# Kernel tuning notes

Hardware: AMD Instinct MI355X
Metric: run time of the kernel (lower is better)

The kernel has to match this reference:

```python
import jax, jax.numpy as jnp
import numpy as np

N_HEAD = 8
C = 32
M_DIM = 256
N_SEQ = 256
L_RES = 384
SQ_C = 1.0 / np.sqrt(C)


def setup_inputs() -> dict:
    key = jax.random.key(0)
    ks = jax.random.split(key, 10)
    hc = N_HEAD * C
    s = 0.02
    return {
        "m": jax.random.normal(ks[0], (N_SEQ, L_RES, M_DIM), dtype=jnp.float32),
        "ln_gamma": jnp.ones((M_DIM,), jnp.float32),
        "ln_beta": jnp.zeros((M_DIM,), jnp.float32),
        "Wq": jax.random.normal(ks[1], (M_DIM, hc), jnp.float32) * s,
        "Wk": jax.random.normal(ks[2], (M_DIM, hc), jnp.float32) * s,
        "Wv": jax.random.normal(ks[3], (M_DIM, hc), jnp.float32) * s,
        "Wg": jax.random.normal(ks[4], (M_DIM, hc), jnp.float32) * s,
        "bg": jnp.zeros((hc,), jnp.float32),
        "Wo": jax.random.normal(ks[5], (hc, M_DIM), jnp.float32) * s,
        "bo": jnp.zeros((M_DIM,), jnp.float32),
    }


def layer_norm(x, gamma, beta, eps=1e-5):
    mu = jnp.mean(x, axis=-1, keepdims=True)
    var = jnp.var(x, axis=-1, keepdims=True)
    return (x - mu) * jax.lax.rsqrt(var + eps) * gamma + beta


def reference(m, ln_gamma, ln_beta, Wq, Wk, Wv, Wg, bg, Wo, bo):
    N, L, D = m.shape
    x = layer_norm(m, ln_gamma, ln_beta)
    q = (x @ Wq).reshape(N, L, N_HEAD, C)
    k = (x @ Wk).reshape(N, L, N_HEAD, C)
    v = (x @ Wv).reshape(N, L, N_HEAD, C)
    g = jax.nn.sigmoid(x @ Wg + bg).reshape(N, L, N_HEAD, C)
    # attention over the sequence axis (s,t), independent per column l, head h
    att = jnp.einsum('slhc,tlhc->stlh', q, k) * SQ_C
    att = jax.nn.softmax(att, axis=1)
    o = jnp.einsum('stlh,tlhc->slhc', att, v) * g
    return o.reshape(N, L, N_HEAD * C) @ Wo + bo
```

## Files before the change

### kernel.cpp

```cpp
#include <hip/hip_runtime.h>
#include <cstdint>
#include <cstddef>

#define NSEQ 256
#define LRES 384
#define MDIM 256
#define NHEAD 8
#define CDIM 32
#define NL (NSEQ*LRES)
#define SQC 0.17677669529663687f

#define X_OFF    0u
#define WT_OFF   25165824u
#define QKVG_OFF 25493504u
#define PROJ_SZ  25165824u
#define O_OFF    (QKVG_OFF + 4u*PROJ_SZ)

typedef __attribute__((ext_vector_type(8))) __bf16 bf16x8;
typedef __attribute__((ext_vector_type(4))) float f32x4;

__device__ __forceinline__ unsigned short f2bf(float f) {
  unsigned int u = __float_as_uint(f);
  u = (u + 0x7FFFu + ((u >> 16) & 1u)) >> 16;
  return (unsigned short)u;
}
__device__ __forceinline__ unsigned short f2bf_fast(float f) {
  return (unsigned short)((__float_as_uint(f) + 0x8000u) >> 16);
}
__device__ __forceinline__ float bf2f(unsigned short u){ return __uint_as_float(((unsigned int)u) << 16); }

__global__ __launch_bounds__(256) void ln_kernel(const float* __restrict__ m,
    const float* __restrict__ gamma, const float* __restrict__ beta,
    unsigned short* __restrict__ x)
{
  int row  = blockIdx.x*4 + (threadIdx.x >> 6);
  int lane = threadIdx.x & 63;
  const float4 v = ((const float4*)(m + (size_t)row*MDIM))[lane];
  float s  = v.x + v.y + v.z + v.w;
  float ss = v.x*v.x + v.y*v.y + v.z*v.z + v.w*v.w;
  #pragma unroll
  for (int off = 32; off > 0; off >>= 1) {
    s  += __shfl_xor(s,  off, 64);
    ss += __shfl_xor(ss, off, 64);
  }
  float mu   = s * (1.f/MDIM);
  float var  = ss * (1.f/MDIM) - mu*mu;
  float rstd = rsqrtf(var + 1e-5f);
  float4 gm = ((const float4*)gamma)[lane];
  float4 bt = ((const float4*)beta)[lane];
  ushort4 pk;
  pk.x = f2bf((v.x - mu)*rstd*gm.x + bt.x);
  pk.y = f2bf((v.y - mu)*rstd*gm.y + bt.y);
  pk.z = f2bf((v.z - mu)*rstd*gm.z + bt.z);
  pk.w = f2bf((v.w - mu)*rstd*gm.w + bt.w);
  ((ushort4*)(x + (size_t)row*MDIM))[lane] = pk;
}

__global__ __launch_bounds__(256) void wtr_kernel(
    const float* __restrict__ W0, const float* __restrict__ W1,
    const float* __restrict__ W2, const float* __restrict__ W3,
    const float* __restrict__ W4, unsigned short* __restrict__ wT)
{
  int p = blockIdx.z;
  const float* W = (p==0)?W0:(p==1)?W1:(p==2)?W2:(p==3)?W3:W4;
  __shared__ float tile[32][33];
  int tx = threadIdx.x & 31, ty0 = threadIdx.x >> 5;
  int bi = blockIdx.x*32, bj = blockIdx.y*32;
  #pragma unroll
  for (int r = 0; r < 4; r++) {
    int ty = ty0 + r*8;
    tile[ty][tx] = W[(bi + ty)*MDIM + bj + tx];
  }
  __syncthreads();
  #pragma unroll
  for (int r = 0; r < 4; r++) {
    int ty = ty0 + r*8;
    wT[p*65536 + (bj + ty)*MDIM + bi + tx] = f2bf(tile[tx][ty]);
  }
}

__global__ __launch_bounds__(256) void proj_kernel(const unsigned short* __restrict__ x,
    const unsigned short* __restrict__ wT, const float* __restrict__ bg,
    unsigned short* __restrict__ qkvg)
{
  __shared__ __align__(16) unsigned short As[128*32];
  __shared__ __align__(16) unsigned short Bs[64*32];
  const int bn = blockIdx.x, bm = blockIdx.y;
  const int tid = threadIdx.x;
  const int lane = tid & 63, wave = tid >> 6;
  const int ln = lane & 15, quad = lane >> 4;
  const int wm = (wave >> 1)*64, wn = (wave & 1)*32;
  const int Rbase = bm*128, Nbase = bn*64;
  const uint4* xg = (const uint4*)x;
  const uint4* wg = (const uint4*)wT;
  uint4* Asv = (uint4*)As;
  uint4* Bsv = (uint4*)Bs;
  const int aRow0 = tid >> 2, aCol = tid & 3;
  const int J0 = Nbase + (tid >> 2);
  const int bIdxBase = (J0 >> 8)*8192 + (J0 & 255)*32 + (tid & 3);

  f32x4 zero = {0.f, 0.f, 0.f, 0.f};
  f32x4 acc[4][2];
  #pragma unroll
  for (int i=0;i<4;i++)
    #pragma unroll
    for (int j=0;j<2;j++) acc[i][j] = zero;

  for (int kk = 0; kk < 8; kk++) {
    Asv[tid]       = xg[(Rbase + aRow0)*32      + kk*4 + aCol];
    Asv[tid + 256] = xg[(Rbase + aRow0 + 64)*32 + kk*4 + aCol];
    Bsv[tid]       = wg[bIdxBase + kk*4];
    __syncthreads();
    bf16x8 af[4], bf[2];
    #pragma unroll
    for (int i=0;i<4;i++) af[i] = __builtin_bit_cast(bf16x8, Asv[(wm + i*16 + ln)*4 + quad]);
    #pragma unroll
    for (int j=0;j<2;j++) bf[j] = __builtin_bit_cast(bf16x8, Bsv[(wn + j*16 + ln)*4 + quad]);
    #pragma unroll
    for (int i=0;i<4;i++)
      #pragma unroll
      for (int j=0;j<2;j++)
        acc[i][j] = __builtin_amdgcn_mfma_f32_16x16x32_bf16(af[i], bf[j], acc[i][j], 0, 0, 0);
    __syncthreads();
  }

  const int p = Nbase >> 8;
  const int sIdx = Rbase / 384;
  const int l0 = Rbase - sIdx*384;
  unsigned short* dstBase = qkvg + (size_t)p*PROJ_SZ;
  #pragma unroll
  for (int i=0;i<4;i++) {
    #pragma unroll
    for (int j=0;j<2;j++) {
      int Jc = Nbase + wn + j*16 + ln;
      int j256 = Jc & 255;
      int h = j256 >> 5, c = j256 & 31;
      #pragma unroll
      for (int r=0;r<4;r++) {
        int row = wm + i*16 + quad*4 + r;
        int lcol = l0 + row;
        float val = acc[i][j][r];
        if (p == 3) val = 1.f/(1.f + __expf(-(val + bg[j256])));
        dstBase[(size_t)((lcol*8 + h)*256 + sIdx)*32 + c] = f2bf(val);
      }
    }
  }
}

__global__ __launch_bounds__(256) void vtr_kernel(const unsigned short* __restrict__ v,
    unsigned short* __restrict__ vt)
{
  __shared__ unsigned short tile[32][33];
  const int lh = blockIdx.y, st = blockIdx.x;
  const unsigned short* src = v  + (size_t)lh*8192;
  unsigned short*       dst = vt + (size_t)lh*8192;
  int tx = threadIdx.x & 31, ty0 = threadIdx.x >> 5;
  #pragma unroll
  for (int r=0;r<4;r++) {
    int ty = ty0 + r*8;
    tile[ty][tx] = src[(st*32 + ty)*32 + tx];
  }
  __syncthreads();
  #pragma unroll
  for (int r=0;r<4;r++) {
    int ty = ty0 + r*8;
    dst[ty*256 + st*32 + tx] = tile[tx][ty];
  }
}

__global__ __launch_bounds__(256, 2) void attn_kernel(
    const unsigned short* __restrict__ qkvg,
    const unsigned short* __restrict__ vt,
    unsigned short* __restrict__ o)
{
  const int h = blockIdx.x, l = blockIdx.y;
  const int tid = threadIdx.x;
  const int wave = tid >> 6, lane = tid & 63;
  const int ln = lane & 15, qd = lane >> 4;
  __shared__ __align__(16) unsigned short Pa[16384];
  const size_t tb = (size_t)(l*8 + h) * 8192;
  const uint4* qg = (const uint4*)qkvg + (tb >> 3);
  const uint4* kg = (const uint4*)(qkvg + (size_t)PROJ_SZ) + (tb >> 3);
  const uint4* vg = (const uint4*)vt + (tb >> 3);
  const int s0 = wave*64;
  const int sw = ln & 7;

  bf16x8 qf[4];
  #pragma unroll
  for (int nj=0;nj<4;nj++)
    qf[nj] = __builtin_bit_cast(bf16x8, qg[(s0 + ln + 16*nj)*4 + qd]);

  f32x4 zero = {0.f,0.f,0.f,0.f};
  f32x4 Oacc[2][4];
  #pragma unroll
  for (int mi=0;mi<2;mi++)
    #pragma unroll
    for (int nj=0;nj<4;nj++) Oacc[mi][nj] = zero;
  float rs[4] = {0.f,0.f,0.f,0.f};

  ushort4* Paw = (ushort4*)Pa;
  const uint4* Pa4 = (const uint4*)Pa;
  const int wbw = wave*1024;
  const int wb4 = wave*512;

  for (int c = 0; c < 4; c++) {
    bf16x8 kf[4];
    uint4 vfr[2][2];
    #pragma unroll
    for (int mi=0;mi<4;mi++)
      kf[mi] = __builtin_bit_cast(bf16x8, kg[(c*64 + 16*mi + ln)*4 + qd]);
    #pragma unroll
    for (int mi=0;mi<2;mi++)
      #pragma unroll
      for (int ks=0;ks<2;ks++)
        vfr[mi][ks] = vg[(ln + 16*mi)*32 + c*8 + ks*4 + qd];

    #pragma unroll
    for (int nj=0;nj<4;nj++) {
      f32x4 sv[4];
      #pragma unroll
      for (int mi=0;mi<4;mi++)
        sv[mi] = __builtin_amdgcn_mfma_f32_16x16x32_bf16(kf[mi], qf[nj], zero, 0, 0, 0);
      const int srow = ln + 16*nj;
      #pragma unroll
      for (int mi=0;mi<4;mi++) {
        float p0 = __expf(sv[mi][0]*SQC);
        float p1 = __expf(sv[mi][1]*SQC);
        float p2 = __expf(sv[mi][2]*SQC);
        float p3 = __expf(sv[mi][3]*SQC);
        rs[nj] += (p0+p1)+(p2+p3);
        ushort4 pk;
        pk.x = f2bf_fast(p0); pk.y = f2bf_fast(p1);
        pk.z = f2bf_fast(p2); pk.w = f2bf_fast(p3);
        Paw[wbw + srow*16 + (((2*mi + (qd>>1)) ^ sw) << 1) + (qd & 1)] = pk;
      }
    }
    #pragma unroll
    for (int ks=0;ks<2;ks++) {
      bf16x8 pf[4];
      #pragma unroll
      for (int nj=0;nj<4;nj++)
        pf[nj] = __builtin_bit_cast(bf16x8, Pa4[wb4 + (ln + 16*nj)*8 + ((4*ks + qd) ^ sw)]);
      #pragma unroll
      for (int mi=0;mi<2;mi++)
        #pragma unroll
        for (int nj=0;nj<4;nj++)
          Oacc[mi][nj] = __builtin_amdgcn_mfma_f32_16x16x32_bf16(
              __builtin_bit_cast(bf16x8, vfr[mi][ks]), pf[nj], Oacc[mi][nj], 0, 0, 0);
    }
  }

  #pragma unroll
  for (int nj=0;nj<4;nj++) {
    float r = rs[nj];
    r += __shfl_xor(r, 16, 64);
    r += __shfl_xor(r, 32, 64);
    rs[nj] = 1.f / r;
  }

  const unsigned short* gg = qkvg + 3u*(size_t)PROJ_SZ + tb;
  #pragma unroll
  for (int mi=0;mi<2;mi++) {
    #pragma unroll
    for (int nj=0;nj<4;nj++) {
      const int sg = s0 + ln + 16*nj;
      const int c0 = 16*mi + 4*qd;
      ushort4 gv = *(const ushort4*)(gg + sg*32 + c0);
      float inv = rs[nj];
      float o0 = Oacc[mi][nj][0] * inv * bf2f(gv.x);
      float o1 = Oacc[mi][nj][1] * inv * bf2f(gv.y);
      float o2 = Oacc[mi][nj][2] * inv * bf2f(gv.z);
      float o3 = Oacc[mi][nj][3] * inv * bf2f(gv.w);
      ushort4 ov;
      ov.x = f2bf(o0); ov.y = f2bf(o1); ov.z = f2bf(o2); ov.w = f2bf(o3);
      *(ushort4*)(o + ((size_t)(sg*LRES + l)*8 + h)*32 + c0) = ov;
    }
  }
}

__global__ __launch_bounds__(256) void out_kernel(const unsigned short* __restrict__ o,
    const unsigned short* __restrict__ wT, const float* __restrict__ bo,
    float* __restrict__ out)
{
  __shared__ __align__(16) unsigned short As[128*32];
  __shared__ __align__(16) unsigned short Bs[64*32];
  const int bn = blockIdx.x, bm = blockIdx.y;
  const int tid = threadIdx.x;
  const int lane = tid & 63, wave = tid >> 6;
  const int ln = lane & 15, quad = lane >> 4;
  const int wm = (wave >> 1)*64, wn = (wave & 1)*32;
  const int Rbase = bm*128, Nbase = bn*64;
  const uint4* og = (const uint4*)o;
  const uint4* wg = (const uint4*)wT;
  uint4* Asv = (uint4*)As;
  uint4* Bsv = (uint4*)Bs;
  const int aRow0 = tid >> 2, aCol = tid & 3;
  const int J0 = Nbase + (tid >> 2);
  const int bIdxBase = 32768 + J0*32 + (tid & 3);

  f32x4 zero = {0.f, 0.f, 0.f, 0.f};
  f32x4 acc[4][2];
  #pragma unroll
  for (int i=0;i<4;i++)
    #pragma unroll
    for (int j=0;j<2;j++) acc[i][j] = zero;

  for (int kk = 0; kk < 8; kk++) {
    Asv[tid]       = og[(Rbase + aRow0)*32      + kk*4 + aCol];
    Asv[tid + 256] = og[(Rbase + aRow0 + 64)*32 + kk*4 + aCol];
    Bsv[tid]       = wg[bIdxBase + kk*4];
    __syncthreads();
    bf16x8 af[4], bf[2];
    #pragma unroll
    for (int i=0;i<4;i++) af[i] = __builtin_bit_cast(bf16x8, Asv[(wm + i*16 + ln)*4 + quad]);
    #pragma unroll
    for (int j=0;j<2;j++) bf[j] = __builtin_bit_cast(bf16x8, Bsv[(wn + j*16 + ln)*4 + quad]);
    #pragma unroll
    for (int i=0;i<4;i++)
      #pragma unroll
      for (int j=0;j<2;j++)
        acc[i][j] = __builtin_amdgcn_mfma_f32_16x16x32_bf16(af[i], bf[j], acc[i][j], 0, 0, 0);
    __syncthreads();
  }

  #pragma unroll
  for (int i=0;i<4;i++) {
    #pragma unroll
    for (int j=0;j<2;j++) {
      int Jc = Nbase + wn + j*16 + ln;
      float bias = bo[Jc];
      #pragma unroll
      for (int r=0;r<4;r++) {
        int row = wm + i*16 + quad*4 + r;
        out[(size_t)(Rbase + row)*256 + Jc] = acc[i][j][r] + bias;
      }
    }
  }
}

extern "C" void kernel_launch(void* const* d_in, const int* in_sizes, int n_in,
                              void* d_out, int out_size, void* d_ws, size_t ws_size,
                              hipStream_t stream)
{
  const float* m     = (const float*)d_in[0];
  const float* gamma = (const float*)d_in[1];
  const float* beta  = (const float*)d_in[2];
  const float* Wq    = (const float*)d_in[3];
  const float* Wk    = (const float*)d_in[4];
  const float* Wv    = (const float*)d_in[5];
  const float* Wg    = (const float*)d_in[6];
  const float* bg    = (const float*)d_in[7];
  const float* Wo    = (const float*)d_in[8];
  const float* bo    = (const float*)d_in[9];
  float* out = (float*)d_out;
  unsigned short* ws   = (unsigned short*)d_ws;
  unsigned short* x    = ws + X_OFF;
  unsigned short* wT   = ws + WT_OFF;
  unsigned short* qkvg = ws + QKVG_OFF;
  unsigned short* ob   = ws + O_OFF;
  unsigned short* vnat = qkvg + 2u*(size_t)PROJ_SZ;

  hipLaunchKernelGGL(ln_kernel,   dim3(NL/4),      dim3(256), 0, stream, m, gamma, beta, x);
  hipLaunchKernelGGL(wtr_kernel,  dim3(8, 8, 5),   dim3(256), 0, stream, Wq, Wk, Wv, Wg, Wo, wT);
  hipLaunchKernelGGL(proj_kernel, dim3(16, 768),   dim3(256), 0, stream, x, wT, bg, qkvg);
  hipLaunchKernelGGL(vtr_kernel,  dim3(8, 3072),   dim3(256), 0, stream, vnat, x);
  hipLaunchKernelGGL(attn_kernel, dim3(8, 384),    dim3(256), 0, stream, qkvg, x, ob);
  hipLaunchKernelGGL(out_kernel,  dim3(4, 768),    dim3(256), 0, stream, ob, wT, bo, out);
}
```

Baseline: 483.7 us.

## Enlarge GEMM tiles with direct global-to-LDS loads and row-major projection output

The projection and output GEMMs move to 128x128 tiles with a K-step of 64, loading through global_load_lds into an XOR-swizzled LDS layout instead of staging through registers. The projection now writes Q/K/V/G in natural row-major order rather than scattering into a per-(l,h) layout. The V transpose and attention kernels gather strided rows from that layout instead. The attention grid is reordered so adjacent blocks share the same head. This aims to cut GEMM load overhead and the scattered projection stores, at the cost of strided, less coalesced reads in attention.

```diff
diff --git a/kernel.cpp b/kernel.cpp
--- a/kernel.cpp
+++ b/kernel.cpp
@@ -28,6 +28,12 @@
   return (unsigned short)((__float_as_uint(f) + 0x8000u) >> 16);
 }
 __device__ __forceinline__ float bf2f(unsigned short u){ return __uint_as_float(((unsigned int)u) << 16); }
+
+__device__ __forceinline__ void gld16(const void* g, void* l) {
+  __builtin_amdgcn_global_load_lds(
+      (const __attribute__((address_space(1))) unsigned int*)g,
+      (__attribute__((address_space(3))) unsigned int*)l, 16, 0, 0);
+}
 
 __global__ __launch_bounds__(256) void ln_kernel(const float* __restrict__ m,
     const float* __restrict__ gamma, const float* __restrict__ beta,
@@ -83,65 +89,77 @@
     const unsigned short* __restrict__ wT, const float* __restrict__ bg,
     unsigned short* __restrict__ qkvg)
 {
-  __shared__ __align__(16) unsigned short As[128*32];
-  __shared__ __align__(16) unsigned short Bs[64*32];
+  __shared__ __align__(16) unsigned short As[128*64];
+  __shared__ __align__(16) unsigned short Bs[128*64];
   const int bn = blockIdx.x, bm = blockIdx.y;
   const int tid = threadIdx.x;
   const int lane = tid & 63, wave = tid >> 6;
-  const int ln = lane & 15, quad = lane >> 4;
-  const int wm = (wave >> 1)*64, wn = (wave & 1)*32;
-  const int Rbase = bm*128, Nbase = bn*64;
-  const uint4* xg = (const uint4*)x;
-  const uint4* wg = (const uint4*)wT;
-  uint4* Asv = (uint4*)As;
-  uint4* Bsv = (uint4*)Bs;
-  const int aRow0 = tid >> 2, aCol = tid & 3;
-  const int J0 = Nbase + (tid >> 2);
-  const int bIdxBase = (J0 >> 8)*8192 + (J0 & 255)*32 + (tid & 3);
-
-  f32x4 zero = {0.f, 0.f, 0.f, 0.f};
-  f32x4 acc[4][2];
+  const int ln = lane & 15, qd = lane >> 4;
+  const int wm = (wave >> 1)*64, wn = (wave & 1)*64;
+  const int Rbase = bm*128, Nbase = bn*128;
+
+  const int row0 = tid >> 3;
+  const int kc   = (tid & 7) ^ (row0 & 7);
+  const unsigned short* aS = x + (size_t)(Rbase + row0)*256 + kc*8;
+  const unsigned short* bS = wT + (size_t)(bn >> 1)*65536
+                           + (size_t)((bn & 1)*128 + row0)*256 + kc*8;
+  unsigned short* ldsA = As + wave*512;
+  unsigned short* ldsB = Bs + wave*512;
+
+  f32x4 zero = {0.f,0.f,0.f,0.f};
+  f32x4 acc[4][4];
   #pragma unroll
   for (int i=0;i<4;i++)
     #pragma unroll
-    for (int j=0;j<2;j++) acc[i][j] = zero;
-
-  for (int kk = 0; kk < 8; kk++) {
-    Asv[tid]       = xg[(Rbase + aRow0)*32      + kk*4 + aCol];
-    Asv[tid + 256] = xg[(Rbase + aRow0 + 64)*32 + kk*4 + aCol];
-    Bsv[tid]       = wg[bIdxBase + kk*4];
+    for (int j=0;j<4;j++) acc[i][j] = zero;
+
+  const uint4* As4 = (const uint4*)As;
+  const uint4* Bs4 = (const uint4*)Bs;
+
+  for (int kk = 0; kk < 4; kk++) {
+    #pragma unroll
+    for (int e = 0; e < 4; e++) {
+      gld16(aS + e*8192, ldsA + e*2048);
+      gld16(bS + e*8192, ldsB + e*2048);
+    }
+    aS += 64; bS += 64;
     __syncthreads();
-    bf16x8 af[4], bf[2];
-    #pragma unroll
-    for (int i=0;i<4;i++) af[i] = __builtin_bit_cast(bf16x8, Asv[(wm + i*16 + ln)*4 + quad]);
-    #pragma unroll
-    for (int j=0;j<2;j++) bf[j] = __builtin_bit_cast(bf16x8, Bsv[(wn + j*16 + ln)*4 + quad]);
-    #pragma unroll
-    for (int i=0;i<4;i++)
-      #pragma unroll
-      for (int j=0;j<2;j++)
-        acc[i][j] = __builtin_amdgcn_mfma_f32_16x16x32_bf16(af[i], bf[j], acc[i][j], 0, 0, 0);
+    #pragma unroll
+    for (int kh = 0; kh < 2; kh++) {
+      bf16x8 af[4], bfr[4];
+      #pragma unroll
+      for (int i=0;i<4;i++) {
+        int r = wm + i*16 + ln;
+        af[i] = __builtin_bit_cast(bf16x8, As4[r*8 + ((kh*4 + qd) ^ (r & 7))]);
+      }
+      #pragma unroll
+      for (int j=0;j<4;j++) {
+        int r = wn + j*16 + ln;
+        bfr[j] = __builtin_bit_cast(bf16x8, Bs4[r*8 + ((kh*4 + qd) ^ (r & 7))]);
+      }
+      #pragma unroll
+      for (int i=0;i<4;i++)
+        #pragma unroll
+        for (int j=0;j<4;j++)
+          acc[i][j] = __builtin_amdgcn_mfma_f32_16x16x32_bf16(af[i], bfr[j], acc[i][j], 0, 0, 0);
+    }
     __syncthreads();
   }
 
   const int p = Nbase >> 8;
-  const int sIdx = Rbase / 384;
-  const int l0 = Rbase - sIdx*384;
   unsigned short* dstBase = qkvg + (size_t)p*PROJ_SZ;
   #pragma unroll
   for (int i=0;i<4;i++) {
     #pragma unroll
-    for (int j=0;j<2;j++) {
+    for (int j=0;j<4;j++) {
       int Jc = Nbase + wn + j*16 + ln;
       int j256 = Jc & 255;
-      int h = j256 >> 5, c = j256 & 31;
       #pragma unroll
       for (int r=0;r<4;r++) {
-        int row = wm + i*16 + quad*4 + r;
-        int lcol = l0 + row;
+        int row = Rbase + wm + i*16 + qd*4 + r;
         float val = acc[i][j][r];
         if (p == 3) val = 1.f/(1.f + __expf(-(val + bg[j256])));
-        dstBase[(size_t)((lcol*8 + h)*256 + sIdx)*32 + c] = f2bf(val);
+        dstBase[(size_t)row*256 + j256] = f2bf(val);
       }
     }
   }
@@ -151,20 +169,20 @@
     unsigned short* __restrict__ vt)
 {
   __shared__ unsigned short tile[32][33];
-  const int lh = blockIdx.y, st = blockIdx.x;
-  const unsigned short* src = v  + (size_t)lh*8192;
-  unsigned short*       dst = vt + (size_t)lh*8192;
+  const int st = blockIdx.x;
+  const int lh = blockIdx.y;
+  const int l = lh >> 3, h = lh & 7;
   int tx = threadIdx.x & 31, ty0 = threadIdx.x >> 5;
   #pragma unroll
   for (int r=0;r<4;r++) {
     int ty = ty0 + r*8;
-    tile[ty][tx] = src[(st*32 + ty)*32 + tx];
+    tile[ty][tx] = v[((size_t)(st*32 + ty)*384 + l)*256 + h*32 + tx];
   }
   __syncthreads();
   #pragma unroll
   for (int r=0;r<4;r++) {
     int ty = ty0 + r*8;
-    dst[ty*256 + st*32 + tx] = tile[tx][ty];
+    vt[(size_t)lh*8192 + ty*256 + st*32 + tx] = tile[tx][ty];
   }
 }
 
@@ -173,22 +191,22 @@
     const unsigned short* __restrict__ vt,
     unsigned short* __restrict__ o)
 {
-  const int h = blockIdx.x, l = blockIdx.y;
+  const int l = blockIdx.x, h = blockIdx.y;
   const int tid = threadIdx.x;
   const int wave = tid >> 6, lane = tid & 63;
   const int ln = lane & 15, qd = lane >> 4;
   __shared__ __align__(16) unsigned short Pa[16384];
-  const size_t tb = (size_t)(l*8 + h) * 8192;
-  const uint4* qg = (const uint4*)qkvg + (tb >> 3);
-  const uint4* kg = (const uint4*)(qkvg + (size_t)PROJ_SZ) + (tb >> 3);
-  const uint4* vg = (const uint4*)vt + (tb >> 3);
+  const uint4* qg = (const uint4*)qkvg;
+  const uint4* kg = qg + (size_t)PROJ_SZ/8;
+  const uint4* vg = (const uint4*)vt + (size_t)(l*8 + h)*1024;
+  const int hq = h*4;
   const int s0 = wave*64;
   const int sw = ln & 7;
 
   bf16x8 qf[4];
   #pragma unroll
   for (int nj=0;nj<4;nj++)
-    qf[nj] = __builtin_bit_cast(bf16x8, qg[(s0 + ln + 16*nj)*4 + qd]);
+    qf[nj] = __builtin_bit_cast(bf16x8, qg[((size_t)(s0 + ln + 16*nj)*384 + l)*32 + hq + qd]);
 
   f32x4 zero = {0.f,0.f,0.f,0.f};
   f32x4 Oacc[2][4];
@@ -208,7 +226,7 @@
     uint4 vfr[2][2];
     #pragma unroll
     for (int mi=0;mi<4;mi++)
-      kf[mi] = __builtin_bit_cast(bf16x8, kg[(c*64 + 16*mi + ln)*4 + qd]);
+      kf[mi] = __builtin_bit_cast(bf16x8, kg[((size_t)(c*64 + 16*mi + ln)*384 + l)*32 + hq + qd]);
     #pragma unroll
     for (int mi=0;mi<2;mi++)
       #pragma unroll
@@ -258,22 +276,22 @@
     rs[nj] = 1.f / r;
   }
 
-  const unsigned short* gg = qkvg + 3u*(size_t)PROJ_SZ + tb;
+  const unsigned short* gg = qkvg + 3u*(size_t)PROJ_SZ;
   #pragma unroll
   for (int mi=0;mi<2;mi++) {
     #pragma unroll
     for (int nj=0;nj<4;nj++) {
       const int sg = s0 + ln + 16*nj;
       const int c0 = 16*mi + 4*qd;
-      ushort4 gv = *(const ushort4*)(gg + sg*32 + c0);
+      const size_t rowOff = ((size_t)sg*384 + l)*256 + h*32 + c0;
+      ushort4 gv = *(const ushort4*)(gg + rowOff);
       float inv = rs[nj];
-      float o0 = Oacc[mi][nj][0] * inv * bf2f(gv.x);
-      float o1 = Oacc[mi][nj][1] * inv * bf2f(gv.y);
-      float o2 = Oacc[mi][nj][2] * inv * bf2f(gv.z);
-      float o3 = Oacc[mi][nj][3] * inv * bf2f(gv.w);
       ushort4 ov;
-      ov.x = f2bf(o0); ov.y = f2bf(o1); ov.z = f2bf(o2); ov.w = f2bf(o3);
-      *(ushort4*)(o + ((size_t)(sg*LRES + l)*8 + h)*32 + c0) = ov;
+      ov.x = f2bf(Oacc[mi][nj][0] * inv * bf2f(gv.x));
+      ov.y = f2bf(Oacc[mi][nj][1] * inv * bf2f(gv.y));
+      ov.z = f2bf(Oacc[mi][nj][2] * inv * bf2f(gv.z));
+      ov.w = f2bf(Oacc[mi][nj][3] * inv * bf2f(gv.w));
+      *(ushort4*)(o + rowOff) = ov;
     }
   }
 }
@@ -282,57 +300,72 @@
     const unsigned short* __restrict__ wT, const float* __restrict__ bo,
     float* __restrict__ out)
 {
-  __shared__ __align__(16) unsigned short As[128*32];
-  __shared__ __align__(16) unsigned short Bs[64*32];
+  __shared__ __align__(16) unsigned short As[128*64];
+  __shared__ __align__(16) unsigned short Bs[128*64];
   const int bn = blockIdx.x, bm = blockIdx.y;
   const int tid = threadIdx.x;
   const int lane = tid & 63, wave = tid >> 6;
-  const int ln = lane & 15, quad = lane >> 4;
-  const int wm = (wave >> 1)*64, wn = (wave & 1)*32;
-  const int Rbase = bm*128, Nbase = bn*64;
-  const uint4* og = (const uint4*)o;
-  const uint4* wg = (const uint4*)wT;
-  uint4* Asv = (uint4*)As;
-  uint4* Bsv = (uint4*)Bs;
-  const int aRow0 = tid >> 2, aCol = tid & 3;
-  const int J0 = Nbase + (tid >> 2);
-  const int bIdxBase = 32768 + J0*32 + (tid & 3);
-
-  f32x4 zero = {0.f, 0.f, 0.f, 0.f};
-  f32x4 acc[4][2];
+  const int ln = lane & 15, qd = lane >> 4;
+  const int wm = (wave >> 1)*64, wn = (wave & 1)*64;
+  const int Rbase = bm*128, Nbase = bn*128;
+
+  const int row0 = tid >> 3;
+  const int kc   = (tid & 7) ^ (row0 & 7);
+  const unsigned short* aS = o  + (size_t)(Rbase + row0)*256 + kc*8;
+  const unsigned short* bS = wT + 4u*65536 + (size_t)(Nbase + row0)*256 + kc*8;
+  unsigned short* ldsA = As + wave*512;
+  unsigned short* ldsB = Bs + wave*512;
+
+  f32x4 zero = {0.f,0.f,0.f,0.f};
+  f32x4 acc[4][4];
   #pragma unroll
   for (int i=0;i<4;i++)
     #pragma unroll
-    for (int j=0;j<2;j++) acc[i][j] = zero;
-
-  for (int kk = 0; kk < 8; kk++) {
-    Asv[tid]       = og[(Rbase + aRow0)*32      + kk*4 + aCol];
-    Asv[tid + 256] = og[(Rbase + aRow0 + 64)*32 + kk*4 + aCol];
-    Bsv[tid]       = wg[bIdxBase + kk*4];
+    for (int j=0;j<4;j++) acc[i][j] = zero;
+
+  const uint4* As4 = (const uint4*)As;
+  const uint4* Bs4 = (const uint4*)Bs;
+
+  for (int kk = 0; kk < 4; kk++) {
+    #pragma unroll
+    for (int e = 0; e < 4; e++) {
+      gld16(aS + e*8192, ldsA + e*2048);
+      gld16(bS + e*8192, ldsB + e*2048);
+    }
+    aS += 64; bS += 64;
     __syncthreads();
-    bf16x8 af[4], bf[2];
-    #pragma unroll
-    for (int i=0;i<4;i++) af[i] = __builtin_bit_cast(bf16x8, Asv[(wm + i*16 + ln)*4 + quad]);
-    #pragma unroll
-    for (int j=0;j<2;j++) bf[j] = __builtin_bit_cast(bf16x8, Bsv[(wn + j*16 + ln)*4 + quad]);
-    #pragma unroll
-    for (int i=0;i<4;i++)
-      #pragma unroll
-      for (int j=0;j<2;j++)
-        acc[i][j] = __builtin_amdgcn_mfma_f32_16x16x32_bf16(af[i], bf[j], acc[i][j], 0, 0, 0);
+    #pragma unroll
+    for (int kh = 0; kh < 2; kh++) {
+      bf16x8 af[4], bfr[4];
+      #pragma unroll
+      for (int i=0;i<4;i++) {
+        int r = wm + i*16 + ln;
+        af[i] = __builtin_bit_cast(bf16x8, As4[r*8 + ((kh*4 + qd) ^ (r & 7))]);
+      }
+      #pragma unroll
+      for (int j=0;j<4;j++) {
+        int r = wn + j*16 + ln;
+        bfr[j] = __builtin_bit_cast(bf16x8, Bs4[r*8 + ((kh*4 + qd) ^ (r & 7))]);
+      }
+      #pragma unroll
+      for (int i=0;i<4;i++)
+        #pragma unroll
+        for (int j=0;j<4;j++)
+          acc[i][j] = __builtin_amdgcn_mfma_f32_16x16x32_bf16(af[i], bfr[j], acc[i][j], 0, 0, 0);
+    }
     __syncthreads();
   }
 
   #pragma unroll
   for (int i=0;i<4;i++) {
     #pragma unroll
-    for (int j=0;j<2;j++) {
+    for (int j=0;j<4;j++) {
       int Jc = Nbase + wn + j*16 + ln;
       float bias = bo[Jc];
       #pragma unroll
       for (int r=0;r<4;r++) {
-        int row = wm + i*16 + quad*4 + r;
-        out[(size_t)(Rbase + row)*256 + Jc] = acc[i][j][r] + bias;
+        int row = Rbase + wm + i*16 + qd*4 + r;
+        out[(size_t)row*256 + Jc] = acc[i][j][r] + bias;
       }
     }
   }
@@ -362,8 +395,8 @@
 
   hipLaunchKernelGGL(ln_kernel,   dim3(NL/4),      dim3(256), 0, stream, m, gamma, beta, x);
   hipLaunchKernelGGL(wtr_kernel,  dim3(8, 8, 5),   dim3(256), 0, stream, Wq, Wk, Wv, Wg, Wo, wT);
-  hipLaunchKernelGGL(proj_kernel, dim3(16, 768),   dim3(256), 0, stream, x, wT, bg, qkvg);
+  hipLaunchKernelGGL(proj_kernel, dim3(8, 768),    dim3(256), 0, stream, x, wT, bg, qkvg);
   hipLaunchKernelGGL(vtr_kernel,  dim3(8, 3072),   dim3(256), 0, stream, vnat, x);
-  hipLaunchKernelGGL(attn_kernel, dim3(8, 384),    dim3(256), 0, stream, qkvg, x, ob);
-  hipLaunchKernelGGL(out_kernel,  dim3(4, 768),    dim3(256), 0, stream, ob, wT, bo, out);
-}
+  hipLaunchKernelGGL(attn_kernel, dim3(384, 8),    dim3(256), 0, stream, qkvg, x, ob);
+  hipLaunchKernelGGL(out_kernel,  dim3(2, 768),    dim3(256), 0, stream, ob, wT, bo, out);
+}
```

Measured after the change: 494.1 us. +2.2%, slower.
